# Optimization experiments

Measured on AMD Instinct MI355X. Metric: run time of the kernel, lower is better.

The kernel has to match this reference:

```python
import jax, jax.numpy as jnp
import numpy as np

N_NODES = 100000
N_EDGES = 1000000
HIDDEN = 64
NUM_CONVS = 3
EPS = 0.0  # GINEConv eps, not trained


def setup_inputs() -> dict:
    key = jax.random.key(0)
    ks = jax.random.split(key, 8)
    z = jax.random.randint(ks[0], (N_NODES,), 0, 100, dtype=jnp.int32)
    edge_index = jax.random.randint(ks[1], (2, N_EDGES), 0, N_NODES, dtype=jnp.int32)
    edge_attr = jax.random.normal(ks[2], (N_EDGES, HIDDEN), dtype=jnp.float32)
    node_emb = jax.random.normal(ks[3], (100, HIDDEN), dtype=jnp.float32)
    s = 1.0 / np.sqrt(HIDDEN)
    W1 = jax.random.uniform(ks[4], (NUM_CONVS, HIDDEN, HIDDEN), jnp.float32, -s, s)
    b1 = jax.random.uniform(ks[5], (NUM_CONVS, HIDDEN), jnp.float32, -s, s)
    W2 = jax.random.uniform(ks[6], (NUM_CONVS, HIDDEN, HIDDEN), jnp.float32, -s, s)
    b2 = jax.random.uniform(ks[7], (NUM_CONVS, HIDDEN), jnp.float32, -s, s)
    return {"node_emb": node_emb, "W1": W1, "b1": b1, "W2": W2, "b2": b2,
            "edge_attr": edge_attr, "z": z, "edge_index": edge_index}


def reference(node_emb, W1, b1, W2, b2, edge_attr, z, edge_index):
    x = node_emb[z]  # [N, H]
    src = edge_index[0]  # x_j (source, message sender)
    dst = edge_index[1]  # aggregation target i
    n = x.shape[0]
    for i in range(NUM_CONVS):
        # message: relu(x_j + edge_attr), scatter-add to target nodes
        msg = jax.nn.relu(x[src] + edge_attr)          # [E, H]
        agg = jax.ops.segment_sum(msg, dst, num_segments=n)  # [N, H]
        out = agg + (1.0 + EPS) * x
        # 2-layer MLP: Linear -> relu -> Linear (no act on last layer)
        h = jax.nn.relu(out @ W1[i].T + b1[i])
        h = h @ W2[i].T + b2[i]
        if i < NUM_CONVS - 1:
            h = jax.nn.relu(h)  # encoder-level activation between convs
        h = h + x  # short_cut residual
        x = h
    return x
```

## Files before the change

### kernel.cpp

```cpp
#include <hip/hip_runtime.h>

#define N_NODES 100000
#define N_EDGES 1000000
#define HID 64
#define SCAN_B 1024
#define SCAN_NB ((N_NODES + SCAN_B - 1) / SCAN_B)
#define GATHER_BLOCKS ((N_NODES * 16) / 256)
#define HIST_BLOCKS ((N_EDGES + 255) / 256)

typedef __attribute__((ext_vector_type(8))) short short8;
typedef __attribute__((ext_vector_type(4))) float f32x4;

__device__ __forceinline__ unsigned short f2bf(float f) {
    unsigned u = __float_as_uint(f);
    u += 0x7fffu + ((u >> 16) & 1u);
    return (unsigned short)(u >> 16);
}
__device__ __forceinline__ short8 pack8(float4 a, float4 b) {
    short8 r;
    r[0] = (short)f2bf(a.x); r[1] = (short)f2bf(a.y);
    r[2] = (short)f2bf(a.z); r[3] = (short)f2bf(a.w);
    r[4] = (short)f2bf(b.x); r[5] = (short)f2bf(b.y);
    r[6] = (short)f2bf(b.z); r[7] = (short)f2bf(b.w);
    return r;
}
__device__ __forceinline__ short8 ldw(const float* __restrict__ W, int row, int k0) {
    const float4* p = (const float4*)(W + (size_t)row * HID + k0);
    return pack8(p[0], p[1]);
}

__global__ __launch_bounds__(256) void prep_kernel(
    const float* __restrict__ node_emb, const int* __restrict__ z,
    float* __restrict__ x, const int* __restrict__ dst, int* __restrict__ offs)
{
    if (blockIdx.x < GATHER_BLOCKS) {
        int t = blockIdx.x * 256 + threadIdx.x;
        int n = t >> 4, c = t & 15;
        if (n >= N_NODES) return;
        int zi = z[n];
        float4 v = ((const float4*)(node_emb + (size_t)zi * HID))[c];
        ((float4*)(x + (size_t)n * HID))[c] = v;
    } else {
        int e = (blockIdx.x - GATHER_BLOCKS) * 256 + threadIdx.x;
        if (e < N_EDGES) atomicAdd(&offs[dst[e]], 1);
    }
}

__global__ __launch_bounds__(1024) void scan1_kernel(
    int* __restrict__ offs, int* __restrict__ bsum)
{
    __shared__ int wsum[16];
    int tid = threadIdx.x, lane = tid & 63, wid = tid >> 6;
    int i = blockIdx.x * SCAN_B + tid;
    int v = (i < N_NODES) ? offs[i] : 0;
    int s = v;
#pragma unroll
    for (int d = 1; d < 64; d <<= 1) {
        int t = __shfl_up(s, (unsigned)d, 64);
        if (lane >= d) s += t;
    }
    if (lane == 63) wsum[wid] = s;
    __syncthreads();
    if (wid == 0) {
        int w = (lane < 16) ? wsum[lane] : 0;
#pragma unroll
        for (int d = 1; d < 16; d <<= 1) {
            int t = __shfl_up(w, (unsigned)d, 64);
            if (lane >= d) w += t;
        }
        if (lane < 16) wsum[lane] = w;
    }
    __syncthreads();
    int woff = (wid == 0) ? 0 : wsum[wid - 1];
    if (i < N_NODES) offs[i] = woff + s - v;
    if (tid == 1023) bsum[blockIdx.x] = wsum[15];
}

__global__ __launch_bounds__(128) void scan2_kernel(int* __restrict__ bsum)
{
    __shared__ int ws[2];
    int tid = threadIdx.x, lane = tid & 63, wid = tid >> 6;
    int v = (tid < SCAN_NB) ? bsum[tid] : 0;
    int s = v;
#pragma unroll
    for (int d = 1; d < 64; d <<= 1) {
        int t = __shfl_up(s, (unsigned)d, 64);
        if (lane >= d) s += t;
    }
    if (lane == 63) ws[wid] = s;
    __syncthreads();
    int add = (wid == 1) ? ws[0] : 0;
    if (tid < SCAN_NB) bsum[tid] = add + s - v;
}

__global__ __launch_bounds__(1024) void scan3_kernel(
    int* __restrict__ offs, const int* __restrict__ bsum)
{
    int i = blockIdx.x * SCAN_B + threadIdx.x;
    if (i < N_NODES) {
        int v = offs[i] + bsum[blockIdx.x];
        atomicExch(&offs[i], v);
    }
}

__global__ __launch_bounds__(256) void fill_kernel(
    const int* __restrict__ src, const int* __restrict__ dst,
    int* __restrict__ offs, int2* __restrict__ eid2)
{
    int e = blockIdx.x * 256 + threadIdx.x;
    if (e < N_EDGES) {
        int d = dst[e];
        int pos = atomicAdd(&offs[d], 1);
        eid2[pos] = make_int2(e, src[e]);
    }
}

__global__ __launch_bounds__(256) void sort_kernel(
    const int* __restrict__ offs, int2* __restrict__ eid2)
{
    int gt = blockIdx.x * 256 + threadIdx.x;
    int n = gt >> 6;
    int lane = threadIdx.x & 63;
    if (n >= N_NODES) return;
    int start = (n == 0) ? 0 : offs[n - 1];
    int end = offs[n];
    int deg = end - start;
    if (deg <= 1 || deg > 64) return;
    int ke = 0x7fffffff, vs = 0;
    if (lane < deg) { int2 t = eid2[start + lane]; ke = t.x; vs = t.y; }
#pragma unroll
    for (int k = 2; k <= 64; k <<= 1) {
        for (int j = k >> 1; j > 0; j >>= 1) {
            int partner = lane ^ j;
            int ke2 = __shfl(ke, partner, 64);
            int vs2 = __shfl(vs, partner, 64);
            bool up = ((lane & k) == 0);
            bool takemin = ((lane < partner) == up);
            bool sw = takemin ? (ke2 < ke) : (ke2 > ke);
            if (sw) { ke = ke2; vs = vs2; }
        }
    }
    if (lane < deg) eid2[start + lane] = make_int2(ke, vs);
}

__global__ __launch_bounds__(256) void agg_kernel(
    const float* __restrict__ x, const float* __restrict__ ea,
    const int2* __restrict__ eid2, const int* __restrict__ offs,
    float* __restrict__ agg)
{
    int gt = blockIdx.x * 256 + threadIdx.x;
    int n = gt >> 6;
    if (n >= N_NODES) return;
    int lane = threadIdx.x & 63;
    int g = lane >> 4, c4 = lane & 15;
    int nu = __builtin_amdgcn_readfirstlane(n);
    int start = (nu == 0) ? 0 : offs[nu - 1];
    int end = offs[nu];
    int deg = end - start;
    int2 my = make_int2(0, 0);
    if (lane < deg) my = eid2[start + lane];
    float4 acc = make_float4(0.f, 0.f, 0.f, 0.f);
    int dmax = deg < 64 ? deg : 64;
    int iters = (dmax + 3) >> 2;
    for (int j = 0; j < iters; ++j) {
        int k = g + 4 * j;
        int eidx = __shfl(my.x, k, 64);
        int sidx = __shfl(my.y, k, 64);
        if (k < dmax) {
            float4 e4 = ((const float4*)(ea + (size_t)eidx * HID))[c4];
            float4 x4 = ((const float4*)(x + (size_t)sidx * HID))[c4];
            acc.x += fmaxf(x4.x + e4.x, 0.f);
            acc.y += fmaxf(x4.y + e4.y, 0.f);
            acc.z += fmaxf(x4.z + e4.z, 0.f);
            acc.w += fmaxf(x4.w + e4.w, 0.f);
        }
    }
    for (int i = start + 64 + g; i < end; i += 4) {
        int2 p = eid2[i];
        float4 e4 = ((const float4*)(ea + (size_t)p.x * HID))[c4];
        float4 x4 = ((const float4*)(x + (size_t)p.y * HID))[c4];
        acc.x += fmaxf(x4.x + e4.x, 0.f);
        acc.y += fmaxf(x4.y + e4.y, 0.f);
        acc.z += fmaxf(x4.z + e4.z, 0.f);
        acc.w += fmaxf(x4.w + e4.w, 0.f);
    }
    acc.x += __shfl_xor(acc.x, 16, 64);
    acc.y += __shfl_xor(acc.y, 16, 64);
    acc.z += __shfl_xor(acc.z, 16, 64);
    acc.w += __shfl_xor(acc.w, 16, 64);
    acc.x += __shfl_xor(acc.x, 32, 64);
    acc.y += __shfl_xor(acc.y, 32, 64);
    acc.z += __shfl_xor(acc.z, 32, 64);
    acc.w += __shfl_xor(acc.w, 32, 64);
    if (g == 0) ((float4*)(agg + (size_t)n * HID))[c4] = acc;
}

__global__ __launch_bounds__(256) void mlp_kernel(
    const float* __restrict__ agg,
    const float* __restrict__ W1, const float* __restrict__ b1,
    const float* __restrict__ W2, const float* __restrict__ b2,
    float* __restrict__ x, int last_relu)
{
    __shared__ unsigned short hl[4][16][64];
    int tid = threadIdx.x;
    int wid = tid >> 6, lane = tid & 63;
    int g = lane >> 4, c = lane & 15;
    int m0 = (blockIdx.x * 4 + wid) * 16;
    if (m0 >= N_NODES) return;

    const float* arow = agg + (size_t)(m0 + c) * HID;
    const float* xrow = x + (size_t)(m0 + c) * HID;
    short8 af0, af1;
    {
        int k0 = g * 8;
        float4 a0 = *(const float4*)(arow + k0), a1 = *(const float4*)(arow + k0 + 4);
        float4 y0 = *(const float4*)(xrow + k0), y1 = *(const float4*)(xrow + k0 + 4);
        af0 = pack8(make_float4(a0.x + y0.x, a0.y + y0.y, a0.z + y0.z, a0.w + y0.w),
                    make_float4(a1.x + y1.x, a1.y + y1.y, a1.z + y1.z, a1.w + y1.w));
        int k1 = 32 + g * 8;
        float4 b0 = *(const float4*)(arow + k1), b1v = *(const float4*)(arow + k1 + 4);
        float4 z0 = *(const float4*)(xrow + k1), z1 = *(const float4*)(xrow + k1 + 4);
        af1 = pack8(make_float4(b0.x + z0.x, b0.y + z0.y, b0.z + z0.z, b0.w + z0.w),
                    make_float4(b1v.x + z1.x, b1v.y + z1.y, b1v.z + z1.z, b1v.w + z1.w));
    }

    f32x4 a10 = {0.f, 0.f, 0.f, 0.f}, a11 = a10, a12 = a10, a13 = a10;
#define L1(JT, ACC) { \
    short8 w0 = ldw(W1, (JT)*16 + c, g * 8); \
    short8 w1 = ldw(W1, (JT)*16 + c, 32 + g * 8); \
    ACC = __builtin_amdgcn_mfma_f32_16x16x32_bf16(af0, w0, ACC, 0, 0, 0); \
    ACC = __builtin_amdgcn_mfma_f32_16x16x32_bf16(af1, w1, ACC, 0, 0, 0); }
    L1(0, a10) L1(1, a11) L1(2, a12) L1(3, a13)
#undef L1

#define HST(JT, ACC) { float bb = b1[(JT) * 16 + c]; \
    hl[wid][4*g + 0][(JT)*16 + c] = f2bf(fmaxf(ACC[0] + bb, 0.f)); \
    hl[wid][4*g + 1][(JT)*16 + c] = f2bf(fmaxf(ACC[1] + bb, 0.f)); \
    hl[wid][4*g + 2][(JT)*16 + c] = f2bf(fmaxf(ACC[2] + bb, 0.f)); \
    hl[wid][4*g + 3][(JT)*16 + c] = f2bf(fmaxf(ACC[3] + bb, 0.f)); }
    HST(0, a10) HST(1, a11) HST(2, a12) HST(3, a13)
#undef HST

    short8 hf0 = *(const short8*)&hl[wid][c][g * 8];
    short8 hf1 = *(const short8*)&hl[wid][c][32 + g * 8];

    f32x4 a20 = {0.f, 0.f, 0.f, 0.f}, a21 = a20, a22 = a20, a23 = a20;
#define L2(CT, ACC) { \
    short8 w0 = ldw(W2, (CT)*16 + c, g * 8); \
    short8 w1 = ldw(W2, (CT)*16 + c, 32 + g * 8); \
    ACC = __builtin_amdgcn_mfma_f32_16x16x32_bf16(hf0, w0, ACC, 0, 0, 0); \
    ACC = __builtin_amdgcn_mfma_f32_16x16x32_bf16(hf1, w1, ACC, 0, 0, 0); }
    L2(0, a20) L2(1, a21) L2(2, a22) L2(3, a23)
#undef L2

#define EPI(CT, ACC) { float bb = b2[(CT) * 16 + c]; \
    _Pragma("unroll") \
    for (int r = 0; r < 4; ++r) { \
        size_t idx = (size_t)(m0 + 4*g + r) * HID + (CT) * 16 + c; \
        float o = ACC[r] + bb; \
        if (last_relu) o = fmaxf(o, 0.f); \
        x[idx] = o + x[idx]; } }
    EPI(0, a20) EPI(1, a21) EPI(2, a22) EPI(3, a23)
#undef EPI
}

extern "C" void kernel_launch(void* const* d_in, const int* in_sizes, int n_in,
                              void* d_out, int out_size, void* d_ws, size_t ws_size,
                              hipStream_t stream) {
    const float* node_emb = (const float*)d_in[0];
    const float* W1 = (const float*)d_in[1];
    const float* b1 = (const float*)d_in[2];
    const float* W2 = (const float*)d_in[3];
    const float* b2 = (const float*)d_in[4];
    const float* ea = (const float*)d_in[5];
    const int* z = (const int*)d_in[6];
    const int* ei = (const int*)d_in[7];
    const int* src = ei;
    const int* dst = ei + N_EDGES;

    float* x = (float*)d_out;
    float* agg = (float*)d_ws;
    int2* eid2 = (int2*)(agg + (size_t)N_NODES * HID);
    int* offs = (int*)(eid2 + N_EDGES);
    int* bsum = offs + N_NODES;

    const int eb = (N_EDGES + 255) / 256;
    const int nodewave_blocks = (N_NODES * 64) / 256;
    const int mlp_blocks = (N_NODES / 16 + 3) / 4;

    hipMemsetAsync(offs, 0, N_NODES * sizeof(int), stream);
    prep_kernel<<<GATHER_BLOCKS + HIST_BLOCKS, 256, 0, stream>>>(
        node_emb, z, x, dst, offs);
    scan1_kernel<<<SCAN_NB, SCAN_B, 0, stream>>>(offs, bsum);
    scan2_kernel<<<1, 128, 0, stream>>>(bsum);
    scan3_kernel<<<SCAN_NB, SCAN_B, 0, stream>>>(offs, bsum);
    fill_kernel<<<eb, 256, 0, stream>>>(src, dst, offs, eid2);
    sort_kernel<<<nodewave_blocks, 256, 0, stream>>>(offs, eid2);

    for (int conv = 0; conv < 3; ++conv) {
        agg_kernel<<<nodewave_blocks, 256, 0, stream>>>(x, ea, eid2, offs, agg);
        mlp_kernel<<<mlp_blocks, 256, 0, stream>>>(
            agg, W1 + conv * HID * HID, b1 + conv * HID,
            W2 + conv * HID * HID, b2 + conv * HID,
            x, conv < 2 ? 1 : 0);
    }
}
```

Baseline: 803.8 us.

## Fuse aggregation into MLP kernel and cache edge attrs as sorted bf16

```diff
diff --git a/kernel.cpp b/kernel.cpp
--- a/kernel.cpp
+++ b/kernel.cpp
@@ -15,6 +15,9 @@
     unsigned u = __float_as_uint(f);
     u += 0x7fffu + ((u >> 16) & 1u);
     return (unsigned short)(u >> 16);
+}
+__device__ __forceinline__ float bf2f(unsigned short u) {
+    return __uint_as_float((unsigned)u << 16);
 }
 __device__ __forceinline__ short8 pack8(float4 a, float4 b) {
     short8 r;
@@ -143,63 +146,15 @@
     if (lane < deg) eid2[start + lane] = make_int2(ke, vs);
 }
 
-__global__ __launch_bounds__(256) void agg_kernel(
-    const float* __restrict__ x, const float* __restrict__ ea,
-    const int2* __restrict__ eid2, const int* __restrict__ offs,
-    float* __restrict__ agg)
-{
-    int gt = blockIdx.x * 256 + threadIdx.x;
-    int n = gt >> 6;
-    if (n >= N_NODES) return;
-    int lane = threadIdx.x & 63;
-    int g = lane >> 4, c4 = lane & 15;
-    int nu = __builtin_amdgcn_readfirstlane(n);
-    int start = (nu == 0) ? 0 : offs[nu - 1];
-    int end = offs[nu];
-    int deg = end - start;
-    int2 my = make_int2(0, 0);
-    if (lane < deg) my = eid2[start + lane];
-    float4 acc = make_float4(0.f, 0.f, 0.f, 0.f);
-    int dmax = deg < 64 ? deg : 64;
-    int iters = (dmax + 3) >> 2;
-    for (int j = 0; j < iters; ++j) {
-        int k = g + 4 * j;
-        int eidx = __shfl(my.x, k, 64);
-        int sidx = __shfl(my.y, k, 64);
-        if (k < dmax) {
-            float4 e4 = ((const float4*)(ea + (size_t)eidx * HID))[c4];
-            float4 x4 = ((const float4*)(x + (size_t)sidx * HID))[c4];
-            acc.x += fmaxf(x4.x + e4.x, 0.f);
-            acc.y += fmaxf(x4.y + e4.y, 0.f);
-            acc.z += fmaxf(x4.z + e4.z, 0.f);
-            acc.w += fmaxf(x4.w + e4.w, 0.f);
-        }
-    }
-    for (int i = start + 64 + g; i < end; i += 4) {
-        int2 p = eid2[i];
-        float4 e4 = ((const float4*)(ea + (size_t)p.x * HID))[c4];
-        float4 x4 = ((const float4*)(x + (size_t)p.y * HID))[c4];
-        acc.x += fmaxf(x4.x + e4.x, 0.f);
-        acc.y += fmaxf(x4.y + e4.y, 0.f);
-        acc.z += fmaxf(x4.z + e4.z, 0.f);
-        acc.w += fmaxf(x4.w + e4.w, 0.f);
-    }
-    acc.x += __shfl_xor(acc.x, 16, 64);
-    acc.y += __shfl_xor(acc.y, 16, 64);
-    acc.z += __shfl_xor(acc.z, 16, 64);
-    acc.w += __shfl_xor(acc.w, 16, 64);
-    acc.x += __shfl_xor(acc.x, 32, 64);
-    acc.y += __shfl_xor(acc.y, 32, 64);
-    acc.z += __shfl_xor(acc.z, 32, 64);
-    acc.w += __shfl_xor(acc.w, 32, 64);
-    if (g == 0) ((float4*)(agg + (size_t)n * HID))[c4] = acc;
-}
-
-__global__ __launch_bounds__(256) void mlp_kernel(
-    const float* __restrict__ agg,
+template<int FIRST>
+__global__ __launch_bounds__(256) void conv_kernel(
+    const float* __restrict__ x_in, float* __restrict__ x_out,
+    const float* __restrict__ ea, unsigned short* __restrict__ eabs,
+    int* __restrict__ srcs, const int2* __restrict__ eid2,
+    const int* __restrict__ offs,
     const float* __restrict__ W1, const float* __restrict__ b1,
     const float* __restrict__ W2, const float* __restrict__ b2,
-    float* __restrict__ x, int last_relu)
+    int last_relu)
 {
     __shared__ unsigned short hl[4][16][64];
     int tid = threadIdx.x;
@@ -208,21 +163,94 @@
     int m0 = (blockIdx.x * 4 + wid) * 16;
     if (m0 >= N_NODES) return;
 
-    const float* arow = agg + (size_t)(m0 + c) * HID;
-    const float* xrow = x + (size_t)(m0 + c) * HID;
-    short8 af0, af1;
-    {
-        int k0 = g * 8;
-        float4 a0 = *(const float4*)(arow + k0), a1 = *(const float4*)(arow + k0 + 4);
-        float4 y0 = *(const float4*)(xrow + k0), y1 = *(const float4*)(xrow + k0 + 4);
-        af0 = pack8(make_float4(a0.x + y0.x, a0.y + y0.y, a0.z + y0.z, a0.w + y0.w),
-                    make_float4(a1.x + y1.x, a1.y + y1.y, a1.z + y1.z, a1.w + y1.w));
-        int k1 = 32 + g * 8;
-        float4 b0 = *(const float4*)(arow + k1), b1v = *(const float4*)(arow + k1 + 4);
-        float4 z0 = *(const float4*)(xrow + k1), z1 = *(const float4*)(xrow + k1 + 4);
-        af1 = pack8(make_float4(b0.x + z0.x, b0.y + z0.y, b0.z + z0.z, b0.w + z0.w),
-                    make_float4(b1v.x + z1.x, b1v.y + z1.y, b1v.z + z1.z, b1v.w + z1.w));
-    }
+    int start = (m0 == 0) ? 0 : offs[m0 - 1];
+    for (int i = 0; i < 16; ++i) {
+        int n = m0 + i;
+        int end = offs[n];
+        int deg = end - start;
+        float4 acc = make_float4(0.f, 0.f, 0.f, 0.f);
+        int dmax = deg < 64 ? deg : 64;
+        int iters = (dmax + 3) >> 2;
+        if (FIRST) {
+            int2 my = make_int2(0, 0);
+            if (lane < deg) my = eid2[start + lane];
+            for (int j = 0; j < iters; ++j) {
+                int k = g + 4 * j;
+                int eidx = __shfl(my.x, k, 64);
+                int sidx = __shfl(my.y, k, 64);
+                if (k < dmax) {
+                    float4 e4 = ((const float4*)(ea + (size_t)eidx * HID))[c];
+                    ushort4 q;
+                    q.x = f2bf(e4.x); q.y = f2bf(e4.y);
+                    q.z = f2bf(e4.z); q.w = f2bf(e4.w);
+                    *(ushort4*)&eabs[(size_t)(start + k) * HID + c * 4] = q;
+                    if (c == 0) srcs[start + k] = sidx;
+                    float4 x4 = ((const float4*)(x_in + (size_t)sidx * HID))[c];
+                    acc.x += fmaxf(x4.x + e4.x, 0.f);
+                    acc.y += fmaxf(x4.y + e4.y, 0.f);
+                    acc.z += fmaxf(x4.z + e4.z, 0.f);
+                    acc.w += fmaxf(x4.w + e4.w, 0.f);
+                }
+            }
+            for (int t = start + 64 + g; t < end; t += 4) {
+                int2 p = eid2[t];
+                float4 e4 = ((const float4*)(ea + (size_t)p.x * HID))[c];
+                ushort4 q;
+                q.x = f2bf(e4.x); q.y = f2bf(e4.y);
+                q.z = f2bf(e4.z); q.w = f2bf(e4.w);
+                *(ushort4*)&eabs[(size_t)t * HID + c * 4] = q;
+                if (c == 0) srcs[t] = p.y;
+                float4 x4 = ((const float4*)(x_in + (size_t)p.y * HID))[c];
+                acc.x += fmaxf(x4.x + e4.x, 0.f);
+                acc.y += fmaxf(x4.y + e4.y, 0.f);
+                acc.z += fmaxf(x4.z + e4.z, 0.f);
+                acc.w += fmaxf(x4.w + e4.w, 0.f);
+            }
+        } else {
+            int mys = 0;
+            if (lane < deg) mys = srcs[start + lane];
+            for (int j = 0; j < iters; ++j) {
+                int k = g + 4 * j;
+                int sidx = __shfl(mys, k, 64);
+                if (k < dmax) {
+                    ushort4 q = *(const ushort4*)&eabs[(size_t)(start + k) * HID + c * 4];
+                    float4 x4 = ((const float4*)(x_in + (size_t)sidx * HID))[c];
+                    acc.x += fmaxf(x4.x + bf2f(q.x), 0.f);
+                    acc.y += fmaxf(x4.y + bf2f(q.y), 0.f);
+                    acc.z += fmaxf(x4.z + bf2f(q.z), 0.f);
+                    acc.w += fmaxf(x4.w + bf2f(q.w), 0.f);
+                }
+            }
+            for (int t = start + 64 + g; t < end; t += 4) {
+                int sidx = srcs[t];
+                ushort4 q = *(const ushort4*)&eabs[(size_t)t * HID + c * 4];
+                float4 x4 = ((const float4*)(x_in + (size_t)sidx * HID))[c];
+                acc.x += fmaxf(x4.x + bf2f(q.x), 0.f);
+                acc.y += fmaxf(x4.y + bf2f(q.y), 0.f);
+                acc.z += fmaxf(x4.z + bf2f(q.z), 0.f);
+                acc.w += fmaxf(x4.w + bf2f(q.w), 0.f);
+            }
+        }
+        acc.x += __shfl_xor(acc.x, 16, 64);
+        acc.y += __shfl_xor(acc.y, 16, 64);
+        acc.z += __shfl_xor(acc.z, 16, 64);
+        acc.w += __shfl_xor(acc.w, 16, 64);
+        acc.x += __shfl_xor(acc.x, 32, 64);
+        acc.y += __shfl_xor(acc.y, 32, 64);
+        acc.z += __shfl_xor(acc.z, 32, 64);
+        acc.w += __shfl_xor(acc.w, 32, 64);
+        if (g == 0) {
+            float4 xv = ((const float4*)(x_in + (size_t)n * HID))[c];
+            ushort4 q;
+            q.x = f2bf(acc.x + xv.x); q.y = f2bf(acc.y + xv.y);
+            q.z = f2bf(acc.z + xv.z); q.w = f2bf(acc.w + xv.w);
+            *(ushort4*)&hl[wid][i][c * 4] = q;
+        }
+        start = end;
+    }
+
+    short8 af0 = *(const short8*)&hl[wid][c][g * 8];
+    short8 af1 = *(const short8*)&hl[wid][c][32 + g * 8];
 
     f32x4 a10 = {0.f, 0.f, 0.f, 0.f}, a11 = a10, a12 = a10, a13 = a10;
 #define L1(JT, ACC) { \
@@ -259,7 +287,7 @@
         size_t idx = (size_t)(m0 + 4*g + r) * HID + (CT) * 16 + c; \
         float o = ACC[r] + bb; \
         if (last_relu) o = fmaxf(o, 0.f); \
-        x[idx] = o + x[idx]; } }
+        x_out[idx] = o + x_in[idx]; } }
     EPI(0, a20) EPI(1, a21) EPI(2, a22) EPI(3, a23)
 #undef EPI
 }
@@ -279,14 +307,17 @@
     const int* dst = ei + N_EDGES;
 
     float* x = (float*)d_out;
-    float* agg = (float*)d_ws;
-    int2* eid2 = (int2*)(agg + (size_t)N_NODES * HID);
+    unsigned short* eabs = (unsigned short*)d_ws;
+    int* srcs = (int*)(eabs + (size_t)N_EDGES * HID);
+    int2* eid2 = (int2*)(srcs + N_EDGES);
     int* offs = (int*)(eid2 + N_EDGES);
     int* bsum = offs + N_NODES;
+    float* x1 = (float*)(bsum + 128);
+    float* x2 = x1 + (size_t)N_NODES * HID;
 
     const int eb = (N_EDGES + 255) / 256;
     const int nodewave_blocks = (N_NODES * 64) / 256;
-    const int mlp_blocks = (N_NODES / 16 + 3) / 4;
+    const int conv_blocks = (N_NODES / 16 + 3) / 4;
 
     hipMemsetAsync(offs, 0, N_NODES * sizeof(int), stream);
     prep_kernel<<<GATHER_BLOCKS + HIST_BLOCKS, 256, 0, stream>>>(
@@ -297,11 +328,12 @@
     fill_kernel<<<eb, 256, 0, stream>>>(src, dst, offs, eid2);
     sort_kernel<<<nodewave_blocks, 256, 0, stream>>>(offs, eid2);
 
-    for (int conv = 0; conv < 3; ++conv) {
-        agg_kernel<<<nodewave_blocks, 256, 0, stream>>>(x, ea, eid2, offs, agg);
-        mlp_kernel<<<mlp_blocks, 256, 0, stream>>>(
-            agg, W1 + conv * HID * HID, b1 + conv * HID,
-            W2 + conv * HID * HID, b2 + conv * HID,
-            x, conv < 2 ? 1 : 0);
-    }
-}
+    conv_kernel<1><<<conv_blocks, 256, 0, stream>>>(
+        x, x1, ea, eabs, srcs, eid2, offs, W1, b1, W2, b2, 1);
+    conv_kernel<0><<<conv_blocks, 256, 0, stream>>>(
+        x1, x2, ea, eabs, srcs, eid2, offs,
+        W1 + HID * HID, b1 + HID, W2 + HID * HID, b2 + HID, 1);
+    conv_kernel<0><<<conv_blocks, 256, 0, stream>>>(
+        x2, x, ea, eabs, srcs, eid2, offs,
+        W1 + 2 * HID * HID, b1 + 2 * HID, W2 + 2 * HID * HID, b2 + 2 * HID, 0);
+}
```

After: 892.9 us. 1.11x slower.
